# Optimization experiments

Measured on AMD Instinct MI355X. Metric: run time of the kernel, lower is better.

Reference implementation:

```python
import jax, jax.numpy as jnp
import numpy as np

NUCLEIC_ACID_CUTOFF = 30.0
OTHER_CUTOFF = 15.0


def _cdist(x):
    # x: [b, n, 3] -> pairwise euclidean distances [b, n, n]
    sq = jnp.sum(x * x, axis=-1)  # [b, n]
    d2 = sq[:, :, None] + sq[:, None, :] - 2.0 * jnp.einsum('bid,bjd->bij', x, x)
    d2 = jnp.maximum(d2, 0.0)
    # safe sqrt (zero diagonal would produce nan grads otherwise)
    safe = jnp.where(d2 > 0.0, d2, 1.0)
    return jnp.where(d2 > 0.0, jnp.sqrt(safe), 0.0)


def setup_inputs() -> dict:
    key = jax.random.key(0)
    k1, k2, k3, k4, k5 = jax.random.split(key, 5)
    b, n = 2, 4096
    # scale ~10 Angstrom spread so distances straddle the 15/30 cutoffs
    true_coords = jax.random.normal(k1, (b, n, 3), dtype=jnp.float32) * 10.0
    pred_coords = true_coords + jax.random.normal(k2, (b, n, 3), dtype=jnp.float32) * 1.5
    is_dna = jax.random.bernoulli(k3, 0.15, (b, n))
    is_rna = jax.random.bernoulli(k4, 0.15, (b, n))
    coords_mask = jax.random.bernoulli(k5, 0.95, (b, n))
    return {
        'pred_coords': pred_coords,
        'true_coords': true_coords,
        'is_dna': is_dna,
        'is_rna': is_rna,
        'coords_mask': coords_mask,
    }


def reference(pred_coords, true_coords, is_dna, is_rna, coords_mask):
    n = pred_coords.shape[1]
    pred_dists = _cdist(pred_coords)  # [b, n, n]
    true_dists = _cdist(true_coords)  # [b, n, n]
    dist_diff = jnp.abs(true_dists - pred_dists)
    eps = (
        jax.nn.sigmoid(0.5 - dist_diff)
        + jax.nn.sigmoid(1.0 - dist_diff)
        + jax.nn.sigmoid(2.0 - dist_diff)
        + jax.nn.sigmoid(4.0 - dist_diff)
    ) / 4.0

    is_nucleotide = is_dna | is_rna  # [b, n]
    is_nucleotide_pair = is_nucleotide[:, :, None] & is_nucleotide[:, None, :]
    inclusion_radius = jnp.where(
        is_nucleotide_pair,
        true_dists < NUCLEIC_ACID_CUTOFF,
        true_dists < OTHER_CUTOFF,
    )
    not_eye = ~jnp.eye(n, dtype=bool)[None, :, :]
    mask = inclusion_radius & not_eye
    mask = mask & (coords_mask[:, :, None] & coords_mask[:, None, :])

    maskf = mask.astype(eps.dtype)
    lddt_sum = jnp.sum(eps * maskf, axis=(-1, -2))  # [b]
    lddt_count = jnp.sum(maskf, axis=(-1, -2))  # [b]
    lddt = lddt_sum / jnp.maximum(lddt_count, 1.0)
    return 1.0 - jnp.mean(lddt)
```

## Files before the change

kernel.cpp:

```cpp
#include <hip/hip_runtime.h>
#include <hip/hip_bf16.h>


#define NRES 4096
#define NBATCH 2
#define TJ 128
#define NBLOCKS (16 * 32 * NBATCH)

#define CUT15 21.6404256133f
#define CUT30 43.2808512267f

#define S1 66.35420923f
#define S2 678.60880385f
#define S3 2039.58217570f
#define S4 1808.04241445f
#define QP1 16.58855231f
#define QP2 339.30440193f
#define QP3 1529.68663177f
#define QP4 1808.04241445f

#define DIAG_EPS 0.80408219445f
#define LOG2E 1.44269504089f

__global__ void pack_kernel(const float* __restrict__ pred,
                            const float* __restrict__ truec,
                            const int* __restrict__ dna,
                            const int* __restrict__ rna,
                            const int* __restrict__ cm,
                            float4* __restrict__ tp,
                            float4* __restrict__ pp,
                            float* __restrict__ acc)
{
    int idx = blockIdx.x * 256 + threadIdx.x;
    if (idx >= NRES * NBATCH) return;
    float nuc = ((dna[idx] | rna[idx]) != 0) ? 1.0f : 0.0f;
    float cmf = (cm[idx] != 0) ? 1.0f : 0.0f;
    tp[idx] = make_float4(truec[3*idx+0]*LOG2E, truec[3*idx+1]*LOG2E, truec[3*idx+2]*LOG2E, nuc);
    pp[idx] = make_float4(pred[3*idx+0]*LOG2E,  pred[3*idx+1]*LOG2E,  pred[3*idx+2]*LOG2E,  cmf);

    float v = cmf;
    #pragma unroll
    for (int o = 32; o > 0; o >>= 1) v += __shfl_down(v, o, 64);
    if ((threadIdx.x & 63) == 0) atomicAdd(&acc[4 + (idx >> 12)], v);
}

__launch_bounds__(256, 4)
__global__ void lddt_main(const float4* __restrict__ tp,
                          const float4* __restrict__ pp,
                          float* __restrict__ acc,
                          unsigned int* __restrict__ done,
                          float* __restrict__ out)
{
    const int b    = blockIdx.z;
    const int j0   = blockIdx.y * TJ;
    const int i    = blockIdx.x * 256 + threadIdx.x;
    const int base = b * NRES;
    const int tid  = threadIdx.x;

    __shared__ float4 stj[TJ];
    __shared__ float4 spj[TJ];

    if (tid < TJ) stj[tid]      = tp[base + j0 + tid];
    else          spj[tid - TJ] = pp[base + j0 + (tid - TJ)];

    const float4 ti4 = tp[base + i];
    const float4 pi4 = pp[base + i];
    const float tix = ti4.x, tiy = ti4.y, tiz = ti4.z;
    const float pix = pi4.x, piy = pi4.y, piz = pi4.z;
    const bool  cmi  = (pi4.w != 0.0f);
    const bool  nuci = (ti4.w != 0.0f);
    const float cHi = cmi ? (nuci ? CUT30 : CUT15) : -1.0f;
    const float cLo = cmi ? CUT15 : -1.0f;

    __syncthreads();

    float s = 0.0f, c = 0.0f;

    #pragma unroll 4
    for (int k = 0; k < TJ; ++k) {
        const float4 tj = stj[k];
        const float4 pj = spj[k];

        float dx = tix - tj.x, dy = tiy - tj.y, dz = tiz - tj.z;
        float dt = __builtin_amdgcn_sqrtf(dx*dx + dy*dy + dz*dz);
        float ex = pix - pj.x, ey = piy - pj.y, ez = piz - pj.z;
        float dp = __builtin_amdgcn_sqrtf(ex*ex + ey*ey + ez*ez);

        float cutoff = (tj.w != 0.0f) ? cHi : cLo;
        float mf = (dt < cutoff) ? pj.w : 0.0f;

        float t = __builtin_amdgcn_exp2f(-fabsf(dt - dp));
        float Q  = 1.0f + t*(S1 + t*(S2 + t*(S3 + t*S4)));
        float Qp = QP1 + t*(QP2 + t*(QP3 + t*QP4));
        float rq = __builtin_amdgcn_rcpf(Q);

        s += mf * ((t * Qp) * rq);
        c += mf;
    }

    #pragma unroll
    for (int off = 32; off > 0; off >>= 1) {
        s += __shfl_down(s, off, 64);
        c += __shfl_down(c, off, 64);
    }

    __shared__ float red_s[4];
    __shared__ float red_c[4];
    const int wid  = tid >> 6;
    const int lane = tid & 63;
    if (lane == 0) { red_s[wid] = s; red_c[wid] = c; }
    __syncthreads();

    if (tid == 0) {
        float ts = red_s[0] + red_s[1] + red_s[2] + red_s[3];
        float tc = red_c[0] + red_c[1] + red_c[2] + red_c[3];
        atomicAdd(&acc[b], ts);
        atomicAdd(&acc[NBATCH + b], tc);
        __threadfence();
        unsigned int old = atomicAdd(done, 1u);
        if (old == NBLOCKS - 1u) {
            float a0 = __hip_atomic_load(&acc[0], __ATOMIC_ACQUIRE, __HIP_MEMORY_SCOPE_AGENT);
            float a1 = __hip_atomic_load(&acc[1], __ATOMIC_ACQUIRE, __HIP_MEMORY_SCOPE_AGENT);
            float c0 = __hip_atomic_load(&acc[2], __ATOMIC_ACQUIRE, __HIP_MEMORY_SCOPE_AGENT);
            float c1 = __hip_atomic_load(&acc[3], __ATOMIC_ACQUIRE, __HIP_MEMORY_SCOPE_AGENT);
            float M0 = __hip_atomic_load(&acc[4], __ATOMIC_ACQUIRE, __HIP_MEMORY_SCOPE_AGENT);
            float M1 = __hip_atomic_load(&acc[5], __ATOMIC_ACQUIRE, __HIP_MEMORY_SCOPE_AGENT);
            float l0 = (a0 - DIAG_EPS * M0) / fmaxf(c0 - M0, 1.0f);
            float l1 = (a1 - DIAG_EPS * M1) / fmaxf(c1 - M1, 1.0f);
            out[0] = 1.0f - 0.5f * (l0 + l1);
        }
    }
}

extern "C" void kernel_launch(void* const* d_in, const int* in_sizes, int n_in,
                              void* d_out, int out_size, void* d_ws, size_t ws_size,
                              hipStream_t stream) {
    const float* pred  = (const float*)d_in[0];
    const float* truec = (const float*)d_in[1];
    const int*   dna   = (const int*)d_in[2];
    const int*   rna   = (const int*)d_in[3];
    const int*   cmask = (const int*)d_in[4];
    float* out = (float*)d_out;

    char* ws = (char*)d_ws;
    float*        acc  = (float*)ws;
    unsigned int* done = (unsigned int*)(ws + 64);
    float4* tp = (float4*)(ws + 1024);
    float4* pp = (float4*)(ws + 1024 + NBATCH*NRES*16);

    (void)hipMemsetAsync(ws, 0, 128, stream);

    pack_kernel<<<(NRES*NBATCH + 255)/256, 256, 0, stream>>>(pred, truec, dna, rna, cmask, tp, pp, acc);

    dim3 grid(NRES / 256, NRES / TJ, NBATCH);
    lddt_main<<<grid, 256, 0, stream>>>(tp, pp, acc, done, out);
}
```

Before: 53.93 us.

## Exploit pair symmetry to compute only upper-triangular tiles

The pair matrix is symmetric, so blocks whose column tile lies entirely below the diagonal now exit early, and diagonal tiles mask to j > i. The final ratio uses half-counts, which makes the separate diagonal correction and the coords-mask count reduction in the pack kernel unnecessary. This roughly halves the pairwise arithmetic, at the cost of early-exit blocks still launching and touching the completion counter. Diagonal-straddling tiles also pay an extra compare per pair.

```diff
diff --git a/kernel.cpp b/kernel.cpp
--- a/kernel.cpp
+++ b/kernel.cpp
@@ -19,7 +19,6 @@
 #define QP3 1529.68663177f
 #define QP4 1808.04241445f
 
-#define DIAG_EPS 0.80408219445f
 #define LOG2E 1.44269504089f
 
 __global__ void pack_kernel(const float* __restrict__ pred,
@@ -28,8 +27,7 @@
                             const int* __restrict__ rna,
                             const int* __restrict__ cm,
                             float4* __restrict__ tp,
-                            float4* __restrict__ pp,
-                            float* __restrict__ acc)
+                            float4* __restrict__ pp)
 {
     int idx = blockIdx.x * 256 + threadIdx.x;
     if (idx >= NRES * NBATCH) return;
@@ -37,12 +35,27 @@
     float cmf = (cm[idx] != 0) ? 1.0f : 0.0f;
     tp[idx] = make_float4(truec[3*idx+0]*LOG2E, truec[3*idx+1]*LOG2E, truec[3*idx+2]*LOG2E, nuc);
     pp[idx] = make_float4(pred[3*idx+0]*LOG2E,  pred[3*idx+1]*LOG2E,  pred[3*idx+2]*LOG2E,  cmf);
+}
 
-    float v = cmf;
-    #pragma unroll
-    for (int o = 32; o > 0; o >>= 1) v += __shfl_down(v, o, 64);
-    if ((threadIdx.x & 63) == 0) atomicAdd(&acc[4 + (idx >> 12)], v);
-}
+#define K_LOOP(DIAG)                                                        \
+    _Pragma("unroll 4")                                                     \
+    for (int k = 0; k < TJ; ++k) {                                          \
+        const float4 tj = stj[k];                                           \
+        const float4 pj = spj[k];                                           \
+        float dx = tix - tj.x, dy = tiy - tj.y, dz = tiz - tj.z;            \
+        float dt = __builtin_amdgcn_sqrtf(dx*dx + dy*dy + dz*dz);           \
+        float ex = pix - pj.x, ey = piy - pj.y, ez = piz - pj.z;            \
+        float dp = __builtin_amdgcn_sqrtf(ex*ex + ey*ey + ez*ez);           \
+        float cutoff = __builtin_fmaf(tj.w, cHiLo, cLo);                    \
+        float mf = (dt < cutoff) ? pj.w : 0.0f;                             \
+        if (DIAG) mf = (j0 + k > i) ? mf : 0.0f;                            \
+        float t = __builtin_amdgcn_exp2f(-fabsf(dt - dp));                  \
+        float Q  = 1.0f + t*(S1 + t*(S2 + t*(S3 + t*S4)));                  \
+        float Qp = QP1 + t*(QP2 + t*(QP3 + t*QP4));                         \
+        float rq = __builtin_amdgcn_rcpf(Q);                                \
+        s += mf * ((t * Qp) * rq);                                          \
+        c += mf;                                                            \
+    }
 
 __launch_bounds__(256, 4)
 __global__ void lddt_main(const float4* __restrict__ tp,
@@ -51,15 +64,34 @@
                           unsigned int* __restrict__ done,
                           float* __restrict__ out)
 {
-    const int b    = blockIdx.z;
-    const int j0   = blockIdx.y * TJ;
-    const int i    = blockIdx.x * 256 + threadIdx.x;
+    const int b   = blockIdx.z;
+    const int bi  = blockIdx.x;
+    const int cj  = blockIdx.y;
+    const int tid = threadIdx.x;
+
+    if (cj < 2 * bi) {
+        if (tid == 0) {
+            __threadfence();
+            unsigned int old = atomicAdd(done, 1u);
+            if (old == NBLOCKS - 1u) {
+                float a0 = __hip_atomic_load(&acc[0], __ATOMIC_ACQUIRE, __HIP_MEMORY_SCOPE_AGENT);
+                float a1 = __hip_atomic_load(&acc[1], __ATOMIC_ACQUIRE, __HIP_MEMORY_SCOPE_AGENT);
+                float c0 = __hip_atomic_load(&acc[2], __ATOMIC_ACQUIRE, __HIP_MEMORY_SCOPE_AGENT);
+                float c1 = __hip_atomic_load(&acc[3], __ATOMIC_ACQUIRE, __HIP_MEMORY_SCOPE_AGENT);
+                float l0 = a0 / fmaxf(c0, 0.5f);
+                float l1 = a1 / fmaxf(c1, 0.5f);
+                out[0] = 1.0f - 0.5f * (l0 + l1);
+            }
+        }
+        return;
+    }
+
     const int base = b * NRES;
-    const int tid  = threadIdx.x;
+    const int j0   = cj * TJ;
+    const int i    = bi * 256 + tid;
 
     __shared__ float4 stj[TJ];
     __shared__ float4 spj[TJ];
-
     if (tid < TJ) stj[tid]      = tp[base + j0 + tid];
     else          spj[tid - TJ] = pp[base + j0 + (tid - TJ)];
 
@@ -71,32 +103,14 @@
     const bool  nuci = (ti4.w != 0.0f);
     const float cHi = cmi ? (nuci ? CUT30 : CUT15) : -1.0f;
     const float cLo = cmi ? CUT15 : -1.0f;
+    const float cHiLo = cHi - cLo;
 
     __syncthreads();
 
     float s = 0.0f, c = 0.0f;
 
-    #pragma unroll 4
-    for (int k = 0; k < TJ; ++k) {
-        const float4 tj = stj[k];
-        const float4 pj = spj[k];
-
-        float dx = tix - tj.x, dy = tiy - tj.y, dz = tiz - tj.z;
-        float dt = __builtin_amdgcn_sqrtf(dx*dx + dy*dy + dz*dz);
-        float ex = pix - pj.x, ey = piy - pj.y, ez = piz - pj.z;
-        float dp = __builtin_amdgcn_sqrtf(ex*ex + ey*ey + ez*ez);
-
-        float cutoff = (tj.w != 0.0f) ? cHi : cLo;
-        float mf = (dt < cutoff) ? pj.w : 0.0f;
-
-        float t = __builtin_amdgcn_exp2f(-fabsf(dt - dp));
-        float Q  = 1.0f + t*(S1 + t*(S2 + t*(S3 + t*S4)));
-        float Qp = QP1 + t*(QP2 + t*(QP3 + t*QP4));
-        float rq = __builtin_amdgcn_rcpf(Q);
-
-        s += mf * ((t * Qp) * rq);
-        c += mf;
-    }
+    if (cj <= 2 * bi + 1) { K_LOOP(1) }
+    else                  { K_LOOP(0) }
 
     #pragma unroll
     for (int off = 32; off > 0; off >>= 1) {
@@ -123,10 +137,8 @@
             float a1 = __hip_atomic_load(&acc[1], __ATOMIC_ACQUIRE, __HIP_MEMORY_SCOPE_AGENT);
             float c0 = __hip_atomic_load(&acc[2], __ATOMIC_ACQUIRE, __HIP_MEMORY_SCOPE_AGENT);
             float c1 = __hip_atomic_load(&acc[3], __ATOMIC_ACQUIRE, __HIP_MEMORY_SCOPE_AGENT);
-            float M0 = __hip_atomic_load(&acc[4], __ATOMIC_ACQUIRE, __HIP_MEMORY_SCOPE_AGENT);
-            float M1 = __hip_atomic_load(&acc[5], __ATOMIC_ACQUIRE, __HIP_MEMORY_SCOPE_AGENT);
-            float l0 = (a0 - DIAG_EPS * M0) / fmaxf(c0 - M0, 1.0f);
-            float l1 = (a1 - DIAG_EPS * M1) / fmaxf(c1 - M1, 1.0f);
+            float l0 = a0 / fmaxf(c0, 0.5f);
+            float l1 = a1 / fmaxf(c1, 0.5f);
             out[0] = 1.0f - 0.5f * (l0 + l1);
         }
     }
@@ -150,7 +162,7 @@
 
     (void)hipMemsetAsync(ws, 0, 128, stream);
 
-    pack_kernel<<<(NRES*NBATCH + 255)/256, 256, 0, stream>>>(pred, truec, dna, rna, cmask, tp, pp, acc);
+    pack_kernel<<<(NRES*NBATCH + 255)/256, 256, 0, stream>>>(pred, truec, dna, rna, cmask, tp, pp);
 
     dim3 grid(NRES / 256, NRES / TJ, NBATCH);
     lddt_main<<<grid, 256, 0, stream>>>(tp, pp, acc, done, out);
```

Result: faster. 50.34 us (-6.7%).
